# Kernel tuning notes

Hardware: AMD Instinct MI355X
Metric: run time of the kernel (lower is better)

## Reference

```python
import jax, jax.numpy as jnp
from jax import lax
import numpy as np

M_RANGE = 2
N_CLASS = 25          # (2*m_range+1)**2 motion classes
IM_CHANNEL = 3        # channels of the last frame


def _conv(x, kernel, m_range):
    # x: [N, n_class, H, W], kernel: [1, n_class, k, k] -> [N, 1, H, W]
    pad = [(m_range, m_range), (m_range, m_range)]
    return lax.conv_general_dilated(
        x, kernel, window_strides=(1, 1), padding=pad,
        dimension_numbers=('NCHW', 'OIHW', 'NCHW'))


def setup_inputs() -> dict:
    key = jax.random.key(0)
    k1, k2, k3 = jax.random.split(key, 3)
    B, H, W = 32, 256, 256
    im_input = jax.random.normal(k1, (B, 2 * IM_CHANNEL, H, W), dtype=jnp.float32)
    m_kernel = jax.random.normal(k2, (1, N_CLASS, 2 * M_RANGE + 1, 2 * M_RANGE + 1), dtype=jnp.float32)
    gt_motion = jax.random.randint(k3, (B, 1, H, W), 0, N_CLASS, dtype=jnp.int32)
    return {'im_input': im_input, 'm_kernel': m_kernel, 'gt_motion': gt_motion}


def reference(im_input, m_kernel, gt_motion):
    B, _, H, W = im_input.shape
    # label2mask: one-hot over motion classes -> [B, n_class, H, W]
    m_mask = jax.nn.one_hot(gt_motion[:, 0], N_CLASS, axis=1, dtype=im_input.dtype)
    # construct_seg: batched conv instead of per-sample loop -> [B, 1, H, W]
    seg = _conv(m_mask, m_kernel, M_RANGE)
    disappear = jax.nn.relu(seg - 1.0)
    appear = jax.nn.relu(1.0 - disappear)
    # construct_image: last im_channel frames, gated by appear
    im = im_input[:, -IM_CHANNEL:] * appear  # appear broadcasts over channel dim
    # per-channel expansion against the motion mask: [B, C, n_class, H, W]
    im_expand = im[:, :, None, :, :] * m_mask[:, None, :, :, :]
    # fold channel dim into batch and run a single batched conv
    pred = _conv(im_expand.reshape(B * IM_CHANNEL, N_CLASS, H, W), m_kernel, M_RANGE)
    pred = pred.reshape(B, IM_CHANNEL, H, W)
    return (pred, m_mask, 1.0 - appear)
```

## Files before the change

kernel.cpp:

```cpp
#include <hip/hip_runtime.h>

#define BB 32
#define H 256
#define W 256
#define NC 25
#define KS 5
#define TILE 32
#define GT_T 40
#define AP_T 36

__global__ __launch_bounds__(256, 4)
void gtnet_fused(const float* __restrict__ im_input,
                 const float* __restrict__ m_kernel,
                 const int* __restrict__ gt,
                 float* __restrict__ out_pred,
                 float* __restrict__ out_mask,
                 float* __restrict__ out_app)
{
    __shared__ __align__(16) int   s_gt[GT_T][GT_T];
    __shared__             float   s_wk[NC * NC + 7];
    __shared__ __align__(16) float s_img[AP_T][AP_T][4];

    const int tid = threadIdx.x;
    const int bx  = blockIdx.x;
    const int tiles_per_row = W / TILE;
    const int tiles_per_img = (H / TILE) * tiles_per_row;
    const int b  = bx / tiles_per_img;
    const int t  = bx % tiles_per_img;
    const int oh = (t / tiles_per_row) * TILE;
    const int ow = (t % tiles_per_row) * TILE;

    for (int i = tid; i < NC * NC; i += 256) s_wk[i] = m_kernel[i];

    const int* gtb = gt + b * (H * W);
    for (int i = tid; i < GT_T * GT_T; i += 256) {
        int y = i / GT_T, x = i % GT_T;
        int gy = oh - 4 + y, gx = ow - 4 + x;
        int v = -1;
        if (gy >= 0 && gy < H && gx >= 0 && gx < W) v = gtb[gy * W + gx];
        s_gt[y][x] = v;
    }
    __syncthreads();

    {
        float* mb = out_mask + (size_t)b * (NC * H * W);
        const int y  = tid >> 3;
        const int x4 = tid & 7;
        const int4 g = *reinterpret_cast<const int4*>(&s_gt[y + 4][4 + 4 * x4]);
        #pragma unroll
        for (int c = 0; c < NC; ++c) {
            float4 v;
            v.x = (g.x == c) ? 1.f : 0.f;
            v.y = (g.y == c) ? 1.f : 0.f;
            v.z = (g.z == c) ? 1.f : 0.f;
            v.w = (g.w == c) ? 1.f : 0.f;
            *reinterpret_cast<float4*>(&mb[(c * H + oh + y) * W + ow + 4 * x4]) = v;
        }
    }

    const float* imb = im_input + ((size_t)b * 6 + 3) * (H * W);
    for (int idx = tid; idx < AP_T * AP_T; idx += 256) {
        int p = idx / AP_T, q = idx % AP_T;
        float seg = 0.f;
        #pragma unroll
        for (int i = 0; i < KS; ++i) {
            #pragma unroll
            for (int j = 0; j < KS; ++j) {
                int cls = s_gt[p + i][q + j];
                seg += (cls >= 0) ? s_wk[cls * NC + i * KS + j] : 0.f;
            }
        }
        float dis = fmaxf(seg - 1.f, 0.f);
        float app = fmaxf(1.f - dis, 0.f);
        int gy = oh - 2 + p, gx = ow - 2 + q;
        float i0 = 0.f, i1 = 0.f, i2 = 0.f;
        if (gy >= 0 && gy < H && gx >= 0 && gx < W) {
            int o = gy * W + gx;
            i0 = imb[o] * app;
            i1 = imb[H * W + o] * app;
            i2 = imb[2 * H * W + o] * app;
        }
        float4 v; v.x = i0; v.y = i1; v.z = i2; v.w = app;
        *reinterpret_cast<float4*>(&s_img[p][q][0]) = v;
    }
    __syncthreads();

    {
        float* ab = out_app + (size_t)b * (H * W);
        #pragma unroll
        for (int k = 0; k < 4; ++k) {
            int idx = k * 256 + tid;
            int y = idx >> 5, x = idx & 31;
            ab[(oh + y) * W + ow + x] = 1.f - s_img[y + 2][x + 2][3];
        }
    }

    {
        const int py = (tid >> 4) << 1;
        const int px = (tid & 15) << 1;
        float2 acc[2][3];
        #pragma unroll
        for (int dy = 0; dy < 2; ++dy)
            #pragma unroll
            for (int ch = 0; ch < 3; ++ch) { acc[dy][ch].x = 0.f; acc[dy][ch].y = 0.f; }

        #pragma unroll
        for (int sy = 0; sy < 6; ++sy) {
            #pragma unroll
            for (int sx = 0; sx < 6; ++sx) {
                int cls = s_gt[py + 2 + sy][px + 2 + sx];
                int cw  = (cls >= 0) ? cls : 0;
                const float4 im4 = *reinterpret_cast<const float4*>(&s_img[py + sy][px + sx][0]);
                #pragma unroll
                for (int dy = 0; dy < 2; ++dy) {
                    const int i = sy - dy;
                    if (i < 0 || i >= KS) continue;
                    #pragma unroll
                    for (int dx = 0; dx < 2; ++dx) {
                        const int j = sx - dx;
                        if (j < 0 || j >= KS) continue;
                        float w = s_wk[cw * NC + i * KS + j];
                        if (dx == 0) {
                            acc[dy][0].x += im4.x * w;
                            acc[dy][1].x += im4.y * w;
                            acc[dy][2].x += im4.z * w;
                        } else {
                            acc[dy][0].y += im4.x * w;
                            acc[dy][1].y += im4.y * w;
                            acc[dy][2].y += im4.z * w;
                        }
                    }
                }
            }
        }
        float* pb = out_pred + (size_t)b * 3 * H * W;
        #pragma unroll
        for (int ch = 0; ch < 3; ++ch)
            #pragma unroll
            for (int dy = 0; dy < 2; ++dy)
                *reinterpret_cast<float2*>(&pb[(ch * H + oh + py + dy) * W + ow + px]) = acc[dy][ch];
    }
}

extern "C" void kernel_launch(void* const* d_in, const int* in_sizes, int n_in,
                              void* d_out, int out_size, void* d_ws, size_t ws_size,
                              hipStream_t stream) {
    const float* im_input = (const float*)d_in[0];
    const float* m_kernel = (const float*)d_in[1];
    const int*   gt       = (const int*)d_in[2];

    float* out_pred = (float*)d_out;
    float* out_mask = out_pred + (size_t)BB * 3 * H * W;
    float* out_app  = out_mask + (size_t)BB * NC * H * W;

    const int blocks = BB * (H / TILE) * (W / TILE);
    gtnet_fused<<<blocks, 256, 0, stream>>>(im_input, m_kernel, gt,
                                            out_pred, out_mask, out_app);
}
```

Before: 317.4 us.

## Switch to wide 8x128 tiles with 1x4 per-thread column outputs

Changes the block tile from 32x32 to 8 rows by 128 columns so each tile row is a longer contiguous run for the mask, appear and pred writes. Each thread now computes a vertical strip of 4 pixels in one column, so the pred stores become fully coalesced scalar rows across the warp. The appear output is written during the halo pass, which removes the separate readback loop. The thin tile enlarges the vertical halo overhead: 12 of 16 gt rows are loaded for 8 output rows, which adds redundant seg/appear computation and global loads.

```diff
diff --git a/kernel.cpp b/kernel.cpp
--- a/kernel.cpp
+++ b/kernel.cpp
@@ -4,12 +4,14 @@
 #define H 256
 #define W 256
 #define NC 25
-#define KS 5
-#define TILE 32
-#define GT_T 40
-#define AP_T 36
+#define TH 8
+#define TW 128
+#define GH 16
+#define GW 136
+#define AH 12
+#define AW 132
 
-__global__ __launch_bounds__(256, 4)
+__global__ __launch_bounds__(256)
 void gtnet_fused(const float* __restrict__ im_input,
                  const float* __restrict__ m_kernel,
                  const int* __restrict__ gt,
@@ -17,24 +19,23 @@
                  float* __restrict__ out_mask,
                  float* __restrict__ out_app)
 {
-    __shared__ __align__(16) int   s_gt[GT_T][GT_T];
-    __shared__             float   s_wk[NC * NC + 7];
-    __shared__ __align__(16) float s_img[AP_T][AP_T][4];
+    __shared__ float s_wk[NC * NC];
+    __shared__ __align__(16) int    s_gt[GH][GW];
+    __shared__ __align__(16) float4 s_img[AH][AW];
 
     const int tid = threadIdx.x;
     const int bx  = blockIdx.x;
-    const int tiles_per_row = W / TILE;
-    const int tiles_per_img = (H / TILE) * tiles_per_row;
+    const int tiles_per_img = (H / TH) * (W / TW);
     const int b  = bx / tiles_per_img;
     const int t  = bx % tiles_per_img;
-    const int oh = (t / tiles_per_row) * TILE;
-    const int ow = (t % tiles_per_row) * TILE;
+    const int oh = (t >> 1) * TH;
+    const int ow = (t & 1) * TW;
 
     for (int i = tid; i < NC * NC; i += 256) s_wk[i] = m_kernel[i];
 
     const int* gtb = gt + b * (H * W);
-    for (int i = tid; i < GT_T * GT_T; i += 256) {
-        int y = i / GT_T, x = i % GT_T;
+    for (int i = tid; i < GH * GW; i += 256) {
+        int y = i / GW, x = i - y * GW;
         int gy = oh - 4 + y, gx = ow - 4 + x;
         int v = -1;
         if (gy >= 0 && gy < H && gx >= 0 && gx < W) v = gtb[gy * W + gx];
@@ -43,10 +44,11 @@
     __syncthreads();
 
     {
-        float* mb = out_mask + (size_t)b * (NC * H * W);
-        const int y  = tid >> 3;
-        const int x4 = tid & 7;
-        const int4 g = *reinterpret_cast<const int4*>(&s_gt[y + 4][4 + 4 * x4]);
+        float* mb = out_mask + (size_t)b * (NC * H * W) + (size_t)oh * W + ow;
+        const int r  = tid >> 5;
+        const int c4 = (tid & 31) * 4;
+        const int4 g = *reinterpret_cast<const int4*>(&s_gt[4 + r][4 + c4]);
+        const size_t ro = (size_t)r * W + c4;
         #pragma unroll
         for (int c = 0; c < NC; ++c) {
             float4 v;
@@ -54,91 +56,74 @@
             v.y = (g.y == c) ? 1.f : 0.f;
             v.z = (g.z == c) ? 1.f : 0.f;
             v.w = (g.w == c) ? 1.f : 0.f;
-            *reinterpret_cast<float4*>(&mb[(c * H + oh + y) * W + ow + 4 * x4]) = v;
+            *reinterpret_cast<float4*>(&mb[(size_t)c * (H * W) + ro]) = v;
         }
     }
 
-    const float* imb = im_input + ((size_t)b * 6 + 3) * (H * W);
-    for (int idx = tid; idx < AP_T * AP_T; idx += 256) {
-        int p = idx / AP_T, q = idx % AP_T;
-        float seg = 0.f;
-        #pragma unroll
-        for (int i = 0; i < KS; ++i) {
+    {
+        const float* imb = im_input + ((size_t)b * 6 + 3) * (H * W);
+        float* ab = out_app + (size_t)b * (H * W);
+        for (int idx = tid; idx < AH * AW; idx += 256) {
+            int p = idx / AW, q = idx - p * AW;
+            float seg = 0.f;
             #pragma unroll
-            for (int j = 0; j < KS; ++j) {
-                int cls = s_gt[p + i][q + j];
-                seg += (cls >= 0) ? s_wk[cls * NC + i * KS + j] : 0.f;
+            for (int i = 0; i < 5; ++i)
+                #pragma unroll
+                for (int j = 0; j < 5; ++j) {
+                    int cls = s_gt[p + i][q + j];
+                    seg += (cls >= 0) ? s_wk[cls * NC + i * 5 + j] : 0.f;
+                }
+            float app = fmaxf(1.f - fmaxf(seg - 1.f, 0.f), 0.f);
+            int gy = oh - 2 + p, gx = ow - 2 + q;
+            float4 v; v.x = 0.f; v.y = 0.f; v.z = 0.f; v.w = app;
+            if (gy >= 0 && gy < H && gx >= 0 && gx < W) {
+                int o = gy * W + gx;
+                v.x = imb[o] * app;
+                v.y = imb[H * W + o] * app;
+                v.z = imb[2 * H * W + o] * app;
             }
+            s_img[p][q] = v;
+            if (p >= 2 && p < 2 + TH && q >= 2 && q < 2 + TW)
+                ab[(size_t)(oh + p - 2) * W + (ow + q - 2)] = 1.f - app;
         }
-        float dis = fmaxf(seg - 1.f, 0.f);
-        float app = fmaxf(1.f - dis, 0.f);
-        int gy = oh - 2 + p, gx = ow - 2 + q;
-        float i0 = 0.f, i1 = 0.f, i2 = 0.f;
-        if (gy >= 0 && gy < H && gx >= 0 && gx < W) {
-            int o = gy * W + gx;
-            i0 = imb[o] * app;
-            i1 = imb[H * W + o] * app;
-            i2 = imb[2 * H * W + o] * app;
-        }
-        float4 v; v.x = i0; v.y = i1; v.z = i2; v.w = app;
-        *reinterpret_cast<float4*>(&s_img[p][q][0]) = v;
     }
     __syncthreads();
 
     {
-        float* ab = out_app + (size_t)b * (H * W);
+        const int x0 = tid & 127;
+        const int y0 = (tid >> 7) * 4;
+        float acc[4][3];
         #pragma unroll
-        for (int k = 0; k < 4; ++k) {
-            int idx = k * 256 + tid;
-            int y = idx >> 5, x = idx & 31;
-            ab[(oh + y) * W + ow + x] = 1.f - s_img[y + 2][x + 2][3];
+        for (int dy = 0; dy < 4; ++dy) {
+            acc[dy][0] = 0.f; acc[dy][1] = 0.f; acc[dy][2] = 0.f;
         }
-    }
-
-    {
-        const int py = (tid >> 4) << 1;
-        const int px = (tid & 15) << 1;
-        float2 acc[2][3];
-        #pragma unroll
-        for (int dy = 0; dy < 2; ++dy)
-            #pragma unroll
-            for (int ch = 0; ch < 3; ++ch) { acc[dy][ch].x = 0.f; acc[dy][ch].y = 0.f; }
 
         #pragma unroll
-        for (int sy = 0; sy < 6; ++sy) {
+        for (int sy = 0; sy < 8; ++sy) {
             #pragma unroll
-            for (int sx = 0; sx < 6; ++sx) {
-                int cls = s_gt[py + 2 + sy][px + 2 + sx];
-                int cw  = (cls >= 0) ? cls : 0;
-                const float4 im4 = *reinterpret_cast<const float4*>(&s_img[py + sy][px + sx][0]);
+            for (int sx = 0; sx < 5; ++sx) {
+                const int p = y0 + sy, q = x0 + sx;
+                const float4 im4 = s_img[p][q];
+                const int cls = s_gt[p + 2][q + 2];
+                const int cw  = (cls >= 0) ? cls * NC : 0;
                 #pragma unroll
-                for (int dy = 0; dy < 2; ++dy) {
+                for (int dy = 0; dy < 4; ++dy) {
                     const int i = sy - dy;
-                    if (i < 0 || i >= KS) continue;
-                    #pragma unroll
-                    for (int dx = 0; dx < 2; ++dx) {
-                        const int j = sx - dx;
-                        if (j < 0 || j >= KS) continue;
-                        float w = s_wk[cw * NC + i * KS + j];
-                        if (dx == 0) {
-                            acc[dy][0].x += im4.x * w;
-                            acc[dy][1].x += im4.y * w;
-                            acc[dy][2].x += im4.z * w;
-                        } else {
-                            acc[dy][0].y += im4.x * w;
-                            acc[dy][1].y += im4.y * w;
-                            acc[dy][2].y += im4.z * w;
-                        }
-                    }
+                    if (i < 0 || i > 4) continue;
+                    const float w = s_wk[cw + i * 5 + sx];
+                    acc[dy][0] += im4.x * w;
+                    acc[dy][1] += im4.y * w;
+                    acc[dy][2] += im4.z * w;
                 }
             }
         }
+
         float* pb = out_pred + (size_t)b * 3 * H * W;
         #pragma unroll
         for (int ch = 0; ch < 3; ++ch)
             #pragma unroll
-            for (int dy = 0; dy < 2; ++dy)
-                *reinterpret_cast<float2*>(&pb[(ch * H + oh + py + dy) * W + ow + px]) = acc[dy][ch];
+            for (int dy = 0; dy < 4; ++dy)
+                pb[(size_t)(ch * H + oh + y0 + dy) * W + ow + x0] = acc[dy][ch];
     }
 }
 
@@ -153,7 +138,7 @@
     float* out_mask = out_pred + (size_t)BB * 3 * H * W;
     float* out_app  = out_mask + (size_t)BB * NC * H * W;
 
-    const int blocks = BB * (H / TILE) * (W / TILE);
+    const int blocks = BB * (H / TH) * (W / TW);
     gtnet_fused<<<blocks, 256, 0, stream>>>(im_input, m_kernel, gt,
                                             out_pred, out_mask, out_app);
 }
```

After: 321.8 us. Within noise of the previous version (+1.4%).
